# Kernel optimization log

Hardware: AMD Instinct MI355X
Metric: run time of the kernel (lower is better)

Reference implementation:

```python
import jax, jax.numpy as jnp
import numpy as np


def conv2d(x, w, b):
    # x: [B,C,H,W], w: [O,I,3,3] 'same' padding, stride 1
    out = jax.lax.conv_general_dilated(
        x, w, window_strides=(1, 1), padding='SAME',
        dimension_numbers=('NCHW', 'OIHW', 'NCHW'))
    return out + b[None, :, None, None]


def gather_for_attn(S, y, u):
    # y: [B,C,H,W], u: [B,S,S] int indices into W -> [B,S*S,H,C]
    B, C, H, W = y.shape
    uu = jnp.clip(u.reshape(B, 1, S * S), 0, W - 1).astype(jnp.int32)
    yf = y.reshape(B, C * H, W)
    g = jnp.take_along_axis(yf, jnp.broadcast_to(uu, (B, C * H, S * S)), axis=2)
    return g.reshape(B, C, H, S * S).transpose(0, 3, 2, 1)


def setup_inputs() -> dict:
    key = jax.random.key(0)
    ks = jax.random.split(key, 12)
    B, C, S = 2, 256, 64
    H, W = 32, 512
    mid, Cz = 128, 128
    sd = 0.05
    inp = {
        'x': jax.random.normal(ks[0], (B, C, S, S), jnp.float32),
        'y': jax.random.normal(ks[1], (B, C, H, W), jnp.float32),
        'z': jax.random.normal(ks[2], (B, Cz, H, W), jnp.float32),
        'u': jax.random.randint(ks[3], (B, S, S), 0, W, jnp.int32),
        'wq1': jax.random.normal(ks[4], (mid, C, 3, 3), jnp.float32) * sd,
        'bq1': jnp.zeros((mid,), jnp.float32),
        'wq2': jax.random.normal(ks[5], (mid, mid, 3, 3), jnp.float32) * sd,
        'bq2': jnp.zeros((mid,), jnp.float32),
        'wk1': jax.random.normal(ks[6], (mid, C, 3, 3), jnp.float32) * sd,
        'bk1': jnp.zeros((mid,), jnp.float32),
        'wk2': jax.random.normal(ks[7], (mid, mid, 3, 3), jnp.float32) * sd,
        'bk2': jnp.zeros((mid,), jnp.float32),
    }
    return inp


def reference(x, y, z, u, wq1, bq1, wq2, bq2, wk1, bk1, wk2, bk2):
    B, C, S, _ = x.shape
    mid = wq1.shape[0]
    scale = mid ** (-0.5)
    # q projection: conv-relu-conv, then flatten spatial -> [B, S*S, mid]
    q = conv2d(jax.nn.relu(conv2d(x, wq1, bq1)), wq2, bq2)
    q = q.reshape(B, mid, S * S).transpose(0, 2, 1)
    # k projection on y, then per-position gather along W -> [B, S*S, H, mid]
    k = conv2d(jax.nn.relu(conv2d(y, wk1, bk1)), wk2, bk2)
    k = gather_for_attn(S, k, u)
    v = gather_for_attn(S, z, u)  # [B, S*S, H, Cz]
    # single query vs H gathered keys; softmax over H
    dot = scale * jnp.einsum('bnc,bnhc->bnh', q, k)
    w = jax.nn.softmax(dot, axis=-1)
    a = jnp.einsum('bnh,bnhc->bnc', w, v)  # [B, S*S, Cz]
    return a
```

## Files before the change

### kernel.cpp

```cpp
#include <hip/hip_runtime.h>


typedef __attribute__((ext_vector_type(8))) _Float16 f16x8;
typedef __attribute__((ext_vector_type(4))) float f32x4;
typedef __attribute__((ext_vector_type(8))) unsigned short us8;
typedef unsigned short u16;

#define MFMA16F(A, B, C) __builtin_amdgcn_mfma_f32_16x16x32_f16((A), (B), (C), 0, 0, 0)


__global__ __launch_bounds__(256) void prep_k(
    const float* __restrict__ x, const float* __restrict__ y,
    const float* __restrict__ z,
    const float* __restrict__ wq1, const float* __restrict__ wq2,
    const float* __restrict__ wk1, const float* __restrict__ wk2,
    u16* __restrict__ pq1, u16* __restrict__ pq2,
    u16* __restrict__ pk1, u16* __restrict__ pk2,
    u16* __restrict__ ypad, u16* __restrict__ xpad,
    u16* __restrict__ t2k, u16* __restrict__ t1q,
    u16* __restrict__ zf16)
{
  __shared__ float tile[32][33];
  const int bid = blockIdx.x;
  const int tid = threadIdx.x;

  if (bid < 384) {
    int t = bid * 256 + tid;
    const float* w; u16* dst; int IC, tt;
    if (t < 32768)      { w = wq1; dst = pq1; IC = 256; tt = t; }
    else if (t < 49152) { w = wq2; dst = pq2; IC = 128; tt = t - 32768; }
    else if (t < 81920) { w = wk1; dst = pk1; IC = 256; tt = t - 49152; }
    else                { w = wk2; dst = pk2; IC = 128; tt = t - 81920; }
    const int oc = tt / IC, ic = tt % IC;
    const int ICB = IC >> 5;
    const int ocl = oc & 31, ocq = oc >> 5;
    const int icb = ic >> 5, icl = ic & 31;
    const int swz = ((ocl << 5) | icl) ^ ((ocl & 7) << 3);
    #pragma unroll
    for (int rs = 0; rs < 9; ++rs) {
      float v = w[(oc * IC + ic) * 9 + rs];
      long base = (long)rs * (ICB * 4096) + (long)icb * 4096
                + (long)ocq * 1024 + swz;
      dst[base] = __builtin_bit_cast(u16, (_Float16)v);
    }
  } else if (bid < 511) {
    long u = (long)(bid - 384) * 256 + tid;
    if (u >= 32448) return;
    u16* p; int ICB, H, W2;
    if (u < 17472)      { p = ypad; ICB = 8; H = 32; W2 = 514; }
    else if (u < 21632) { u -= 17472; p = xpad; ICB = 8; H = 64; W2 = 66; }
    else if (u < 30368) { u -= 21632; p = t2k; ICB = 4; H = 32; W2 = 514; }
    else                { u -= 30368; p = t1q; ICB = 4; H = 64; W2 = 66; }
    const int H2 = H + 2;
    const long rowsN = (long)2 * ICB * 2 * W2;
    long base;
    if (u < rowsN) {
      int w = (int)(u % W2);
      int t2 = (int)(u / W2);
      int tb = t2 & 1, icb = (t2 >> 1) % ICB, b = (t2 >> 1) / ICB;
      int h = tb ? H2 - 1 : 0;
      base = ((((long)b * H2 + h) * ICB + icb) * W2 + w) * 32;
    } else {
      long v = u - rowsN;
      int side = (int)(v & 1);
      long v2 = v >> 1;
      int h = 1 + (int)(v2 % H);
      int icb = (int)((v2 / H) % ICB);
      int b = (int)(v2 / ((long)H * ICB));
      int w = side ? W2 - 1 : 0;
      base = ((((long)b * H2 + h) * ICB + icb) * W2 + w) * 32;
    }
    us8 zz = {0, 0, 0, 0, 0, 0, 0, 0};
    #pragma unroll
    for (int j = 0; j < 4; ++j)
      *reinterpret_cast<us8*>(&p[base + j * 8]) = zz;
  } else {
    const int id = bid - 511;
    const float* src; int C, H, W, wt, cb, bh, mode, H2, W2;
    u16* d16;
    if (id < 8192)       { src = y; C = 256; H = 32; W = 512; wt = id & 15;       cb = (id >> 4) & 7; bh = id >> 7; d16 = ypad; mode = 0; H2 = 34; W2 = 514; }
    else if (id < 10240) { int i2 = id - 8192;  src = x; C = 256; H = 64; W = 64; wt = i2 & 1;  cb = (i2 >> 1) & 7; bh = i2 >> 4; d16 = xpad; mode = 0; H2 = 66; W2 = 66; }
    else                 { int i3 = id - 10240; src = z; C = 128; H = 32; W = 512; wt = i3 & 15; cb = (i3 >> 4) & 3; bh = i3 >> 6; d16 = zf16; mode = 1; H2 = 0; W2 = 0; }
    const int b = bh / H, h = bh % H;
    const int w0 = wt * 32;
    const int tx = tid & 31, ty = tid >> 5;
    #pragma unroll
    for (int k2 = 0; k2 < 4; ++k2) {
      int c = cb * 32 + ty + k2 * 8;
      tile[ty + k2 * 8][tx] = src[(((long)b * C + c) * H + h) * W + w0 + tx];
    }
    __syncthreads();
    const int cp = (tid & 15) * 2;
    const int wl = tid >> 4;
    if (mode == 0) {
      const int ICB = C >> 5;
      #pragma unroll
      for (int half = 0; half < 2; ++half) {
        const int wloc = wl + half * 16;
        unsigned int lo = (unsigned int)__builtin_bit_cast(u16, (_Float16)tile[cp][wloc]);
        unsigned int hi = (unsigned int)__builtin_bit_cast(u16, (_Float16)tile[cp + 1][wloc]);
        long idx = ((((long)b * H2 + h + 1) * ICB + cb) * W2 + (w0 + wloc + 1)) * 32 + cp;
        *reinterpret_cast<unsigned int*>(&d16[idx]) = lo | (hi << 16);
      }
    } else {
      #pragma unroll
      for (int half = 0; half < 2; ++half) {
        const int wloc = wl + half * 16;
        unsigned int lo = (unsigned int)__builtin_bit_cast(u16, (_Float16)tile[cp][wloc]);
        unsigned int hi = (unsigned int)__builtin_bit_cast(u16, (_Float16)tile[cp + 1][wloc]);
        long idx = (((long)b * 32 + h) * 512 + (w0 + wloc)) * 128 + cb * 32 + cp;
        *reinterpret_cast<unsigned int*>(&d16[idx]) = lo | (hi << 16);
      }
    }
  }
}

template<int ICB, int OF16>
__global__ __launch_bounds__(256, 3) void conv_k(
    const u16* __restrict__ inK, const u16* __restrict__ wpkK,
    const float* __restrict__ biasK, u16* __restrict__ outK,
    const u16* __restrict__ inQ, const u16* __restrict__ wpkQ,
    const float* __restrict__ biasQ, u16* __restrict__ outQ)
{
  __shared__ __align__(16) u16 smem[18432];

  const int tid = threadIdx.x;
  const int lane = tid & 63, wv = tid >> 6;
  const int lm = lane & 15, lq = lane >> 4;
  const int bid = blockIdx.x;
  const int wid = (bid & 7) * 80 + (bid >> 3);

  const u16* in; const u16* wpk; const float* bias; u16* outp;
  int IH, IW, w0, hb, b, ocsel;
  if (wid < 512) {
    in = inK; wpk = wpkK; bias = biasK; outp = outK;
    IH = 32; IW = 512;
    b = wid >> 8; hb = ((wid >> 4) & 15) * 2;
    w0 = ((wid >> 1) & 7) * 64; ocsel = wid & 1;
  } else {
    const int qb = wid - 512;
    in = inQ; wpk = wpkQ; bias = biasQ; outp = outQ;
    IH = 64; IW = 64;
    b = qb >> 6; hb = ((qb >> 1) & 31) * 2;
    w0 = 0; ocsel = qb & 1;
  }
  const int H2 = IH + 2, W2 = IW + 2;
  const int rp = wv >> 1;
  const int pxw = (wv & 1) * 32;

  const int aswz0 = (lm * 32 + lq * 8) ^ ((lm & 7) << 3);

  f32x4 acc[4][2];
  #pragma unroll
  for (int mf = 0; mf < 4; ++mf)
    #pragma unroll
    for (int f = 0; f < 2; ++f) acc[mf][f] = (f32x4)0.f;

  for (int icb = 0; icb < ICB; ++icb) {
    __syncthreads();
    #pragma unroll
    for (int c0 = 0; c0 < 9; ++c0) {
      const int c = c0 * 256 + tid;
      const int t16 = c >> 7;
      const int j = (c & 127) * 8;
      const int rs2 = t16 >> 1, tt = t16 & 1;
      *reinterpret_cast<uint4*>(&smem[rs2 * 2048 + tt * 1024 + j]) =
          *reinterpret_cast<const uint4*>(
              wpk + (long)rs2 * (ICB * 4096) + (long)icb * 4096
                  + (ocsel * 2 + tt) * 1024 + j);
    }
    const u16* rb[3];
    #pragma unroll
    for (int r = 0; r < 3; ++r)
      rb[r] = in + ((((long)b * H2 + hb + rp + r) * ICB + icb) * W2 + (w0 + pxw + lm)) * 32
            + lq * 8;
    __syncthreads();

    #pragma unroll
    for (int r = 0; r < 3; ++r)
      #pragma unroll
      for (int s = 0; s < 3; ++s) {
        const int rs = r * 3 + s;
        const f16x8 bb0 = *reinterpret_cast<const f16x8*>(rb[r] + s * 32);
        const f16x8 bb1 = *reinterpret_cast<const f16x8*>(rb[r] + (16 + s) * 32);
        const int base = rs * 2048 + aswz0;
        const f16x8 a0 = *reinterpret_cast<const f16x8*>(&smem[base]);
        const f16x8 a1 = *reinterpret_cast<const f16x8*>(&smem[base + 512]);
        const f16x8 a2 = *reinterpret_cast<const f16x8*>(&smem[base + 1024]);
        const f16x8 a3 = *reinterpret_cast<const f16x8*>(&smem[base + 1536]);
        acc[0][0] = MFMA16F(a0, bb0, acc[0][0]);
        acc[0][1] = MFMA16F(a0, bb1, acc[0][1]);
        acc[1][0] = MFMA16F(a1, bb0, acc[1][0]);
        acc[1][1] = MFMA16F(a1, bb1, acc[1][1]);
        acc[2][0] = MFMA16F(a2, bb0, acc[2][0]);
        acc[2][1] = MFMA16F(a2, bb1, acc[2][1]);
        acc[3][0] = MFMA16F(a3, bb0, acc[3][0]);
        acc[3][1] = MFMA16F(a3, bb1, acc[3][1]);
      }
  }

  __syncthreads();
  u16* st = smem;
  #pragma unroll
  for (int mf = 0; mf < 4; ++mf)
    #pragma unroll
    for (int f = 0; f < 2; ++f)
      #pragma unroll
      for (int reg = 0; reg < 4; ++reg) {
        const int ocl = mf * 16 + lq * 4 + reg;
        const int px = pxw + f * 16 + lm;
        float v = acc[mf][f][reg] + bias[ocsel * 64 + ocl];
        if (OF16) v = fmaxf(v, 0.f);
        st[(rp * 64 + px) * 72 + ocl] = __builtin_bit_cast(u16, (_Float16)v);
      }
  __syncthreads();
  for (int i = tid; i < 1024; i += 256) {
    const int o8 = i & 7;
    const int px = (i >> 3) & 63;
    const int row = i >> 9;
    us8 val = *reinterpret_cast<const us8*>(&st[(row * 64 + px) * 72 + o8 * 8]);
    u16* dst;
    if (OF16)
      dst = outp + ((((long)b * H2 + hb + row + 1) * 4 + ocsel * 2 + (o8 >> 2)) * W2
                    + (w0 + px + 1)) * 32 + (o8 & 3) * 8;
    else
      dst = outp + (((long)b * IH + hb + row) * IW + w0 + px) * 128
          + ocsel * 64 + o8 * 8;
    *reinterpret_cast<us8*>(dst) = val;
  }
}

__global__ __launch_bounds__(128) void attn_k(
    const u16* __restrict__ qf, const u16* __restrict__ kf,
    const u16* __restrict__ zf, const int* __restrict__ u,
    float* __restrict__ out)
{
  constexpr float SCALE = 0.08838834764831845f;
  const int n = blockIdx.x, b = blockIdx.y;
  const int t = threadIdx.x;

  __shared__ float qs[128];
  __shared__ float logit[32];
  __shared__ float el[32];

  int widx = u[b * 4096 + n];
  widx = widx < 0 ? 0 : (widx > 511 ? 511 : widx);

  qs[t] = (float)__builtin_bit_cast(_Float16, qf[((long)b * 4096 + n) * 128 + t]);
  __syncthreads();

  const int h = t >> 2, quad = t & 3;
  const u16* kcol = kf + (((long)b * 32 + h) * 512 + widx) * 128 + quad * 32;
  float p = 0.f;
  #pragma unroll
  for (int j = 0; j < 32; j += 8) {
    f16x8 kv = *reinterpret_cast<const f16x8*>(kcol + j);
    #pragma unroll
    for (int jj = 0; jj < 8; ++jj)
      p = fmaf(qs[quad * 32 + j + jj], (float)kv[jj], p);
  }
  p += __shfl_xor(p, 1);
  p += __shfl_xor(p, 2);
  if (quad == 0) logit[h] = p * SCALE;
  __syncthreads();

  float m = -3.4e38f;
  #pragma unroll
  for (int h2 = 0; h2 < 32; ++h2) m = fmaxf(m, logit[h2]);
  if (t < 32) el[t] = __expf(logit[t] - m);
  __syncthreads();
  float den = 0.f;
  #pragma unroll
  for (int h2 = 0; h2 < 32; ++h2) den += el[h2];

  const u16* zcol = zf + ((long)b * 32 * 512) * 128 + (long)widx * 128 + t;
  float o0 = 0.f, o1 = 0.f, o2 = 0.f, o3 = 0.f;
  #pragma unroll
  for (int h2 = 0; h2 < 32; h2 += 4) {
    o0 = fmaf(el[h2 + 0], (float)__builtin_bit_cast(_Float16, zcol[(long)(h2 + 0) * 512 * 128]), o0);
    o1 = fmaf(el[h2 + 1], (float)__builtin_bit_cast(_Float16, zcol[(long)(h2 + 1) * 512 * 128]), o1);
    o2 = fmaf(el[h2 + 2], (float)__builtin_bit_cast(_Float16, zcol[(long)(h2 + 2) * 512 * 128]), o2);
    o3 = fmaf(el[h2 + 3], (float)__builtin_bit_cast(_Float16, zcol[(long)(h2 + 3) * 512 * 128]), o3);
  }
  out[((long)b * 4096 + n) * 128 + t] = ((o0 + o1) + (o2 + o3)) / den;
}

extern "C" void kernel_launch(void* const* d_in, const int* in_sizes, int n_in,
                              void* d_out, int out_size, void* d_ws, size_t ws_size,
                              hipStream_t stream) {
  const float* x   = (const float*)d_in[0];
  const float* y   = (const float*)d_in[1];
  const float* z   = (const float*)d_in[2];
  const int*   u   = (const int*)  d_in[3];
  const float* wq1 = (const float*)d_in[4];
  const float* bq1 = (const float*)d_in[5];
  const float* wq2 = (const float*)d_in[6];
  const float* bq2 = (const float*)d_in[7];
  const float* wk1 = (const float*)d_in[8];
  const float* bk1 = (const float*)d_in[9];
  const float* wk2 = (const float*)d_in[10];
  const float* bk2 = (const float*)d_in[11];
  float* out = (float*)d_out;
  u16* wsu = (u16*)d_ws;

  u16* ypad  = wsu + 0;
  u16* xpad  = wsu + 8947712;
  u16* t2k   = wsu + 11177984;
  u16* t1q   = wsu + 15651840;
  u16* zf16  = wsu + 16766976;
  u16* k_f16 = wsu + 20961280;
  u16* q_f16 = wsu + 25155584;
  u16* wpk_q1 = wsu + 26204160;
  u16* wpk_q2 = wsu + 26499072;
  u16* wpk_k1 = wsu + 26646528;
  u16* wpk_k2 = wsu + 26941440;

  prep_k<<<dim3(14847), 256, 0, stream>>>(x, y, z, wq1, wq2, wk1, wk2,
                                          wpk_q1, wpk_q2, wpk_k1, wpk_k2,
                                          ypad, xpad, t2k, t1q, zf16);
  conv_k<8, 1><<<dim3(640), 256, 0, stream>>>(
      ypad, wpk_k1, bk1, t2k, xpad, wpk_q1, bq1, t1q);
  conv_k<4, 0><<<dim3(640), 256, 0, stream>>>(
      t2k, wpk_k2, bk2, k_f16, t1q, wpk_q2, bq2, q_f16);
  attn_k<<<dim3(4096, 2), 128, 0, stream>>>(q_f16, k_f16, zf16, u, out);
}
```

Measured before the change: 94.49 us.

## Compute two output rows per wave in conv kernel to reuse weight tiles

```diff
diff --git a/kernel.cpp b/kernel.cpp
--- a/kernel.cpp
+++ b/kernel.cpp
@@ -116,7 +116,7 @@
 }
 
 template<int ICB, int OF16>
-__global__ __launch_bounds__(256, 3) void conv_k(
+__global__ __launch_bounds__(256, 2) void conv_k(
     const u16* __restrict__ inK, const u16* __restrict__ wpkK,
     const float* __restrict__ biasK, u16* __restrict__ outK,
     const u16* __restrict__ inQ, const u16* __restrict__ wpkQ,
@@ -128,33 +128,35 @@
   const int lane = tid & 63, wv = tid >> 6;
   const int lm = lane & 15, lq = lane >> 4;
   const int bid = blockIdx.x;
-  const int wid = (bid & 7) * 80 + (bid >> 3);
+  const int wid = (bid & 7) * 40 + (bid >> 3);
 
   const u16* in; const u16* wpk; const float* bias; u16* outp;
   int IH, IW, w0, hb, b, ocsel;
-  if (wid < 512) {
+  if (wid < 256) {
     in = inK; wpk = wpkK; bias = biasK; outp = outK;
     IH = 32; IW = 512;
-    b = wid >> 8; hb = ((wid >> 4) & 15) * 2;
+    b = wid >> 7; hb = ((wid >> 4) & 7) * 4;
     w0 = ((wid >> 1) & 7) * 64; ocsel = wid & 1;
   } else {
-    const int qb = wid - 512;
+    const int qb = wid - 256;
     in = inQ; wpk = wpkQ; bias = biasQ; outp = outQ;
     IH = 64; IW = 64;
-    b = qb >> 6; hb = ((qb >> 1) & 31) * 2;
+    b = qb >> 5; hb = ((qb >> 1) & 15) * 4;
     w0 = 0; ocsel = qb & 1;
   }
   const int H2 = IH + 2, W2 = IW + 2;
-  const int rp = wv >> 1;
+  const int rp2 = (wv >> 1) * 2;
   const int pxw = (wv & 1) * 32;
 
   const int aswz0 = (lm * 32 + lq * 8) ^ ((lm & 7) << 3);
 
-  f32x4 acc[4][2];
+  f32x4 acc[4][2][2];
   #pragma unroll
   for (int mf = 0; mf < 4; ++mf)
     #pragma unroll
-    for (int f = 0; f < 2; ++f) acc[mf][f] = (f32x4)0.f;
+    for (int jj = 0; jj < 2; ++jj)
+      #pragma unroll
+      for (int f = 0; f < 2; ++f) acc[mf][jj][f] = (f32x4)0.f;
 
   for (int icb = 0; icb < ICB; ++icb) {
     __syncthreads();
@@ -169,11 +171,11 @@
               wpk + (long)rs2 * (ICB * 4096) + (long)icb * 4096
                   + (ocsel * 2 + tt) * 1024 + j);
     }
-    const u16* rb[3];
-    #pragma unroll
-    for (int r = 0; r < 3; ++r)
-      rb[r] = in + ((((long)b * H2 + hb + rp + r) * ICB + icb) * W2 + (w0 + pxw + lm)) * 32
-            + lq * 8;
+    const u16* rb[4];
+    #pragma unroll
+    for (int jr = 0; jr < 4; ++jr)
+      rb[jr] = in + ((((long)b * H2 + hb + rp2 + jr) * ICB + icb) * W2 + (w0 + pxw + lm)) * 32
+             + lq * 8;
     __syncthreads();
 
     #pragma unroll
@@ -181,21 +183,26 @@
       #pragma unroll
       for (int s = 0; s < 3; ++s) {
         const int rs = r * 3 + s;
-        const f16x8 bb0 = *reinterpret_cast<const f16x8*>(rb[r] + s * 32);
-        const f16x8 bb1 = *reinterpret_cast<const f16x8*>(rb[r] + (16 + s) * 32);
+        f16x8 bb[2][2];
+        #pragma unroll
+        for (int jj = 0; jj < 2; ++jj)
+          #pragma unroll
+          for (int f = 0; f < 2; ++f)
+            bb[jj][f] = *reinterpret_cast<const f16x8*>(rb[r + jj] + (f * 16 + s) * 32);
         const int base = rs * 2048 + aswz0;
         const f16x8 a0 = *reinterpret_cast<const f16x8*>(&smem[base]);
         const f16x8 a1 = *reinterpret_cast<const f16x8*>(&smem[base + 512]);
         const f16x8 a2 = *reinterpret_cast<const f16x8*>(&smem[base + 1024]);
         const f16x8 a3 = *reinterpret_cast<const f16x8*>(&smem[base + 1536]);
-        acc[0][0] = MFMA16F(a0, bb0, acc[0][0]);
-        acc[0][1] = MFMA16F(a0, bb1, acc[0][1]);
-        acc[1][0] = MFMA16F(a1, bb0, acc[1][0]);
-        acc[1][1] = MFMA16F(a1, bb1, acc[1][1]);
-        acc[2][0] = MFMA16F(a2, bb0, acc[2][0]);
-        acc[2][1] = MFMA16F(a2, bb1, acc[2][1]);
-        acc[3][0] = MFMA16F(a3, bb0, acc[3][0]);
-        acc[3][1] = MFMA16F(a3, bb1, acc[3][1]);
+        #pragma unroll
+        for (int jj = 0; jj < 2; ++jj)
+          #pragma unroll
+          for (int f = 0; f < 2; ++f) {
+            acc[0][jj][f] = MFMA16F(a0, bb[jj][f], acc[0][jj][f]);
+            acc[1][jj][f] = MFMA16F(a1, bb[jj][f], acc[1][jj][f]);
+            acc[2][jj][f] = MFMA16F(a2, bb[jj][f], acc[2][jj][f]);
+            acc[3][jj][f] = MFMA16F(a3, bb[jj][f], acc[3][jj][f]);
+          }
       }
   }
 
@@ -204,17 +211,20 @@
   #pragma unroll
   for (int mf = 0; mf < 4; ++mf)
     #pragma unroll
-    for (int f = 0; f < 2; ++f)
-      #pragma unroll
-      for (int reg = 0; reg < 4; ++reg) {
-        const int ocl = mf * 16 + lq * 4 + reg;
-        const int px = pxw + f * 16 + lm;
-        float v = acc[mf][f][reg] + bias[ocsel * 64 + ocl];
-        if (OF16) v = fmaxf(v, 0.f);
-        st[(rp * 64 + px) * 72 + ocl] = __builtin_bit_cast(u16, (_Float16)v);
-      }
-  __syncthreads();
-  for (int i = tid; i < 1024; i += 256) {
+    for (int jj = 0; jj < 2; ++jj)
+      #pragma unroll
+      for (int f = 0; f < 2; ++f)
+        #pragma unroll
+        for (int reg = 0; reg < 4; ++reg) {
+          const int ocl = mf * 16 + lq * 4 + reg;
+          const int px = pxw + f * 16 + lm;
+          const int row = rp2 + jj;
+          float v = acc[mf][jj][f][reg] + bias[ocsel * 64 + ocl];
+          if (OF16) v = fmaxf(v, 0.f);
+          st[(row * 64 + px) * 72 + ocl] = __builtin_bit_cast(u16, (_Float16)v);
+        }
+  __syncthreads();
+  for (int i = tid; i < 2048; i += 256) {
     const int o8 = i & 7;
     const int px = (i >> 3) & 63;
     const int row = i >> 9;
@@ -318,9 +328,9 @@
   prep_k<<<dim3(14847), 256, 0, stream>>>(x, y, z, wq1, wq2, wk1, wk2,
                                           wpk_q1, wpk_q2, wpk_k1, wpk_k2,
                                           ypad, xpad, t2k, t1q, zf16);
-  conv_k<8, 1><<<dim3(640), 256, 0, stream>>>(
+  conv_k<8, 1><<<dim3(320), 256, 0, stream>>>(
       ypad, wpk_k1, bk1, t2k, xpad, wpk_q1, bq1, t1q);
-  conv_k<4, 0><<<dim3(640), 256, 0, stream>>>(
+  conv_k<4, 0><<<dim3(320), 256, 0, stream>>>(
       t2k, wpk_k2, bk2, k_f16, t1q, wpk_q2, bq2, q_f16);
   attn_k<<<dim3(4096, 2), 128, 0, stream>>>(q_f16, k_f16, zf16, u, out);
 }
```

New measurement: 103.6 us. +9.7%, slower.
